# Optimization experiments

Hardware: AMD Instinct MI355X
Metric: run time of the kernel (lower is better)

## Reference

```python
import jax, jax.numpy as jnp
import numpy as np
import math

NHEAD = 8
IOU_THR = 0.2
COS_THR = 0.2


def _build_mask(segments, q):
    # segments: [bz, Lq, 2] (center, length); q: [bz, Lq, d]
    c, l = segments[..., 0], segments[..., 1]
    s, e = c - l / 2, c + l / 2  # ml2se: midpoint-length -> start-end
    inter = jnp.clip(jnp.minimum(e[:, :, None], e[:, None, :])
                     - jnp.maximum(s[:, :, None], s[:, None, :]), 0.0)
    union = l[:, :, None] + l[:, None, :] - inter
    iou = inter / union  # [bz, Lq, Lq]
    qn = q / jnp.maximum(jnp.linalg.norm(q, axis=-1, keepdims=True), 1e-8)
    cos = jnp.einsum('bid,bjd->bij', qn, qn)
    Lq = q.shape[1]
    adj = jnp.broadcast_to(jnp.eye(Lq, dtype=bool), iou.shape)
    adj = jnp.where(iou <= IOU_THR, True, adj)   # adj_matrix[iou<=0.2]=1
    adj = jnp.where(cos <= COS_THR, False, adj)  # adj_matrix[cos<=0.2]=0
    return ~adj  # True = masked


def setup_inputs() -> dict:
    key = jax.random.key(0)
    ks = jax.random.split(key, 8)
    Lq, bz, d = 1024, 8, 512
    bound = 1.0 / math.sqrt(d)
    query = jax.random.normal(ks[0], (Lq, bz, d), jnp.float32)
    segments = jax.random.uniform(ks[1], (bz, Lq, 2), jnp.float32)
    Wq = jax.random.uniform(ks[2], (d, d), jnp.float32, -bound, bound)
    bq = jax.random.uniform(ks[3], (d,), jnp.float32, -bound, bound)
    Wk = jax.random.uniform(ks[4], (d, d), jnp.float32, -bound, bound)
    bk = jax.random.uniform(ks[5], (d,), jnp.float32, -bound, bound)
    Wv = jax.random.uniform(ks[6], (d, d), jnp.float32, -bound, bound)
    bv = jax.random.uniform(ks[7], (d,), jnp.float32, -bound, bound)
    return dict(query=query, segments=segments, Wq=Wq, bq=bq, Wk=Wk, bk=bk,
                Wv=Wv, bv=bv)


def reference(query, segments, Wq, bq, Wk, bk, Wv, bv):
    Lq, bz, d = query.shape
    dh = d // NHEAD
    h = jnp.transpose(query, (1, 0, 2))  # [bz, Lq, d]
    mask = _build_mask(segments, h)      # [bz, Lq, Lq], bool
    Q = (h @ Wq.T + bq).reshape(bz, Lq, NHEAD, dh)
    K = (h @ Wk.T + bk).reshape(bz, Lq, NHEAD, dh)
    V = (h @ Wv.T + bv).reshape(bz, Lq, NHEAD, dh)
    scores = jnp.einsum('bihd,bjhd->bhij', Q, K) / math.sqrt(dh)
    scores = jnp.where(mask[:, None, :, :], -jnp.inf, scores)
    attn = jax.nn.softmax(scores, axis=-1)
    out = jnp.einsum('bhij,bjhd->bihd', attn, V).reshape(bz, Lq, d) + h
    return jnp.transpose(out, (1, 0, 2))  # [Lq, bz, d]
```

## Files before the change

### kernel.cpp

```cpp
#include <hip/hip_runtime.h>
#include <math.h>

#define LQ 1024
#define BZ 8
#define D  512
#define NH 8
#define DH 64
#define IOU_THR 0.2f
#define COS_THR 0.2f
#define NEG (-1e30f)
#define FIXCAP 16384

typedef short bf16x8 __attribute__((ext_vector_type(8)));
typedef float f32x4  __attribute__((ext_vector_type(4)));

#define MFMA16(a, b, cacc) __builtin_amdgcn_mfma_f32_16x16x32_bf16(a, b, cacc, 0, 0, 0)

__device__ inline unsigned short f2bf(float x) {
    union { float f; unsigned int u; } v; v.f = x;
    unsigned int r = v.u + 0x7FFF + ((v.u >> 16) & 1);
    return (unsigned short)(r >> 16);
}

__global__ __launch_bounds__(256) void prep_kernel(const float* __restrict__ query,
                                                   const float* __restrict__ Wq,
                                                   const float* __restrict__ Wk,
                                                   const float* __restrict__ Wv,
                                                   unsigned short* __restrict__ hi,
                                                   unsigned short* __restrict__ Wb,
                                                   float* __restrict__ rnorm) {
    int blk = blockIdx.x, tid = threadIdx.x;
    if (blk < 2048) {
        int w = tid >> 6, lane = tid & 63;
        int row = blk * 4 + w;
        int b = row >> 10, i = row & 1023;
        const float* src = query + ((size_t)i * BZ + b) * D + lane * 8;
        float4 v0 = *(const float4*)src;
        float4 v1 = *(const float4*)(src + 4);
        uint4 pk;
        pk.x = (unsigned)f2bf(v0.x) | ((unsigned)f2bf(v0.y) << 16);
        pk.y = (unsigned)f2bf(v0.z) | ((unsigned)f2bf(v0.w) << 16);
        pk.z = (unsigned)f2bf(v1.x) | ((unsigned)f2bf(v1.y) << 16);
        pk.w = (unsigned)f2bf(v1.z) | ((unsigned)f2bf(v1.w) << 16);
        *(uint4*)(hi + (size_t)row * D + lane * 8) = pk;
        float ss = v0.x * v0.x + v0.y * v0.y + v0.z * v0.z + v0.w * v0.w
                 + v1.x * v1.x + v1.y * v1.y + v1.z * v1.z + v1.w * v1.w;
        #pragma unroll
        for (int s = 1; s < 64; s <<= 1) ss += __shfl_xor(ss, s);
        if (lane == 0) rnorm[row] = 1.0f / fmaxf(sqrtf(ss), 1e-8f);
    } else {
        int t = (blk - 2048) * 256 + tid;
        int mat = t >> 16;
        int off = (t & 65535) * 4;
        const float* src = (mat == 0) ? Wq : (mat == 1) ? Wk : Wv;
        float4 v = *(const float4*)(src + off);
        uint2 p;
        p.x = (unsigned)f2bf(v.x) | ((unsigned)f2bf(v.y) << 16);
        p.y = (unsigned)f2bf(v.z) | ((unsigned)f2bf(v.w) << 16);
        *(uint2*)(Wb + (size_t)mat * D * D + off) = p;
    }
}

__global__ __launch_bounds__(256) void gemm_kernel(const unsigned short* __restrict__ hi,
                                                   const unsigned short* __restrict__ Wb,
                                                   const float* __restrict__ rnorm,
                                                   const float* __restrict__ segments,
                                                   const float* __restrict__ bq,
                                                   const float* __restrict__ bk,
                                                   const float* __restrict__ bv,
                                                   unsigned char* __restrict__ mask,
                                                   unsigned char* __restrict__ summ,
                                                   int* __restrict__ fix_cnt,
                                                   unsigned int* __restrict__ fix_list,
                                                   unsigned short* __restrict__ Qb,
                                                   unsigned short* __restrict__ Kb,
                                                   unsigned short* __restrict__ Vt) {
    __shared__ short As[2][128 * 32], Bs[2][128 * 32];
    __shared__ float4 iSE[128], jSE[128];
    __shared__ int summ_lds[8][2], summ_t_lds[8][2];
    int blk = blockIdx.x, tid = threadIdx.x, w = tid >> 6, lane = tid & 63;
    int c = lane & 15, q4 = lane >> 4;
    int wr = w >> 1, wc = w & 1;

    bool is_qkv = blk < 768;
    const char *Asrc, *Bsrc;
    int b = 0, i0 = 0, j0 = 0, z = 0, m0 = 0, n0 = 0;
    if (is_qkv) {
        z = blk >> 8; int rem = blk & 255;
        m0 = (rem >> 2) * 128; n0 = (rem & 3) * 128;
        Asrc = (const char*)(hi + (size_t)m0 * D);
        Bsrc = (const char*)(Wb + (size_t)z * D * D + (size_t)n0 * D);
    } else {
        int id2 = blk - 768;
        b = id2 / 36;
        int t = id2 - b * 36;
        int it = 0;
        while (t >= 8 - it) { t -= 8 - it; it++; }
        int jt = it + t;
        i0 = it * 128; j0 = jt * 128;
        Asrc = (const char*)(hi + ((size_t)b * LQ + i0) * D);
        Bsrc = (const char*)(hi + ((size_t)b * LQ + j0) * D);
        if (tid < 16) {
            summ_lds[tid >> 1][tid & 1] = 0;
            summ_t_lds[tid >> 1][tid & 1] = 0;
        }
    }

    int lrow = lane >> 2;
    int gl   = (lane & 3) ^ ((lane >> 3) & 3);
    size_t goff = (size_t)lrow * 1024 + (size_t)gl * 16;
    int lds_off = lrow * 64 + (lane & 3) * 16;

    uint4 ra[2], rb[2];
    #pragma unroll
    for (int m = 0; m < 2; m++) {
        int n = 2 * w + m;
        ra[m] = *(const uint4*)(Asrc + (size_t)n * 16384 + goff);
        rb[m] = *(const uint4*)(Bsrc + (size_t)n * 16384 + goff);
    }
    #pragma unroll
    for (int m = 0; m < 2; m++) {
        int n = 2 * w + m;
        *(uint4*)((char*)As[0] + n * 1024 + lds_off) = ra[m];
        *(uint4*)((char*)Bs[0] + n * 1024 + lds_off) = rb[m];
    }
    __syncthreads();

    f32x4 acc[4][4] = {};
    int rswz = (c >> 1) & 3;
    for (int k = 0; k < 16; k++) {
        int cur = k & 1;
        if (k < 15) {
            size_t kb = (size_t)(k + 1) * 64;
            #pragma unroll
            for (int m = 0; m < 2; m++) {
                int n = 2 * w + m;
                ra[m] = *(const uint4*)(Asrc + kb + (size_t)n * 16384 + goff);
                rb[m] = *(const uint4*)(Bsrc + kb + (size_t)n * 16384 + goff);
            }
        }
        bf16x8 af[4], bf[4];
        #pragma unroll
        for (int f = 0; f < 4; f++) {
            af[f] = *(const bf16x8*)&As[cur][(wr * 64 + f * 16 + c) * 32 + (q4 ^ rswz) * 8];
            bf[f] = *(const bf16x8*)&Bs[cur][(wc * 64 + f * 16 + c) * 32 + (q4 ^ rswz) * 8];
        }
        #pragma unroll
        for (int fr = 0; fr < 4; fr++)
            #pragma unroll
            for (int fc = 0; fc < 4; fc++)
                acc[fr][fc] = MFMA16(af[fr], bf[fc], acc[fr][fc]);
        if (k < 15) {
            int nxt = cur ^ 1;
            #pragma unroll
            for (int m = 0; m < 2; m++) {
                int n = 2 * w + m;
                *(uint4*)((char*)As[nxt] + n * 1024 + lds_off) = ra[m];
                *(uint4*)((char*)Bs[nxt] + n * 1024 + lds_off) = rb[m];
            }
        }
        __syncthreads();
    }

    if (is_qkv) {
        const float* bias = (z == 0) ? bq : (z == 1) ? bk : bv;
        #pragma unroll
        for (int fr = 0; fr < 4; fr++)
            #pragma unroll
            for (int r = 0; r < 4; r++) {
                int m = m0 + wr * 64 + fr * 16 + q4 * 4 + r;
                int bb = m >> 10, i = m & 1023;
                #pragma unroll
                for (int fc = 0; fc < 4; fc++) {
                    int n = n0 + wc * 64 + fc * 16 + c;
                    unsigned short us = f2bf(acc[fr][fc][r] + bias[n]);
                    int hh = n >> 6, dh = n & 63;
                    size_t bh = (size_t)bb * NH + hh;
                    if (z == 2)
                        Vt[(bh * DH + dh) * LQ + i] = us;
                    else {
                        unsigned short* dst = (z == 0) ? Qb : Kb;
                        dst[(bh * LQ + i) * DH + dh] = us;
                    }
                }
            }
    } else {
        const float2* seg2 = (const float2*)(segments + (size_t)b * LQ * 2);
        const float* rn = rnorm + b * LQ;
        if (tid < 128) {
            float2 cl = seg2[i0 + tid];
            iSE[tid] = make_float4(cl.x - cl.y * 0.5f, cl.x + cl.y * 0.5f, cl.y, rn[i0 + tid]);
        } else {
            float2 cl = seg2[j0 + tid - 128];
            jSE[tid - 128] = make_float4(cl.x - cl.y * 0.5f, cl.x + cl.y * 0.5f, cl.y, rn[j0 + tid - 128]);
        }
        __syncthreads();

        bool offdiag = (i0 != j0);
        unsigned char* mbase = mask + ((size_t)b << 20);
        int anyT[4] = {0, 0, 0, 0};
        #pragma unroll
        for (int fr = 0; fr < 4; fr++) {
            int anyun = 0;
            unsigned int tpack[4] = {0, 0, 0, 0};
            #pragma unroll
            for (int r = 0; r < 4; r++) {
                int il = wr * 64 + fr * 16 + q4 * 4 + r;
                int i = i0 + il;
                float4 I = iSE[il];
                #pragma unroll
                for (int fc = 0; fc < 4; fc++) {
                    int jl = wc * 64 + fc * 16 + c;
                    int j = j0 + jl;
                    float4 J = jSE[jl];
                    float cosv = acc[fr][fc][r] * I.w * J.w;
                    if (fabsf(cosv - COS_THR) < 1.5e-3f) {
                        int idx = atomicAdd(fix_cnt, 1);
                        if (idx < FIXCAP)
                            fix_list[idx] = ((unsigned int)b << 20) | ((unsigned int)i << 10) | j;
                    }
                    float inter = fmaxf(fminf(I.y, J.y) - fmaxf(I.x, J.x), 0.0f);
                    float uni   = I.z + J.z - inter;
                    float iou   = inter / uni;
                    bool adj = ((iou <= IOU_THR) || (i == j)) && (cosv > COS_THR);
                    mbase[(size_t)i * LQ + j] = adj ? 0 : 1;
                    tpack[fc] |= (adj ? 0u : 1u) << (8 * r);
                    anyun |= adj ? 1 : 0;
                    anyT[fc] |= adj ? 1 : 0;
                }
            }
            if (anyun) atomicOr(&summ_lds[wr * 4 + fr][wc], 1);
            if (offdiag) {
                int ibase = i0 + wr * 64 + fr * 16 + q4 * 4;
                #pragma unroll
                for (int fc = 0; fc < 4; fc++) {
                    int j = j0 + wc * 64 + fc * 16 + c;
                    *(unsigned int*)&mbase[(size_t)j * LQ + ibase] = tpack[fc];
                }
            }
        }
        if (offdiag) {
            #pragma unroll
            for (int fc = 0; fc < 4; fc++)
                if (anyT[fc]) atomicOr(&summ_t_lds[wc * 4 + fc][wr], 1);
        }
        __syncthreads();
        if (tid < 16) {
            int lit = tid >> 1, ljt = tid & 1;
            summ[((size_t)b * 64 + (i0 >> 4) + lit) * 16 + (j0 >> 6) + ljt] =
                summ_lds[lit][ljt] ? 1 : 0;
            if (offdiag)
                summ[((size_t)b * 64 + (j0 >> 4) + lit) * 16 + (i0 >> 6) + ljt] =
                    summ_t_lds[lit][ljt] ? 1 : 0;
        }
    }
}

__global__ __launch_bounds__(64) void fixup_kernel(const float* __restrict__ query,
                                                   const float* __restrict__ rnorm,
                                                   const float* __restrict__ segments,
                                                   const int* __restrict__ fix_cnt,
                                                   const unsigned int* __restrict__ fix_list,
                                                   unsigned char* __restrict__ mask,
                                                   unsigned char* __restrict__ summ) {
    int cnt = *fix_cnt; if (cnt > FIXCAP) cnt = FIXCAP;
    int lane = threadIdx.x;
    for (int e = blockIdx.x; e < cnt; e += gridDim.x) {
        unsigned int pk = fix_list[e];
        int b = pk >> 20, i = (pk >> 10) & 1023, j = pk & 1023;
        const float* hri = query + ((size_t)i * BZ + b) * D;
        const float* hrj = query + ((size_t)j * BZ + b) * D;
        double dd = 0.0;
        #pragma unroll
        for (int k = 0; k < D / 64; k++)
            dd += (double)hri[k * 64 + lane] * (double)hrj[k * 64 + lane];
        #pragma unroll
        for (int s = 1; s < 64; s <<= 1) dd += __shfl_xor(dd, s);
        if (lane == 0) {
            float rni = rnorm[b * LQ + i], rnj = rnorm[b * LQ + j];
            float cosv = (float)(dd * (double)rni * (double)rnj);
            const float* seg = segments + (size_t)b * LQ * 2;
            float ci = seg[i * 2], li = seg[i * 2 + 1];
            float cj = seg[j * 2], lj = seg[j * 2 + 1];
            float si = ci - li * 0.5f, ei = ci + li * 0.5f;
            float sj = cj - lj * 0.5f, ej = cj + lj * 0.5f;
            float inter = fmaxf(fminf(ei, ej) - fmaxf(si, sj), 0.0f);
            float iou = inter / (li + lj - inter);
            bool adj = ((iou <= IOU_THR) || (i == j)) && (cosv > COS_THR);
            unsigned char mv = adj ? 0 : 1;
            mask[((size_t)b * LQ + i) * LQ + j] = mv;
            mask[((size_t)b * LQ + j) * LQ + i] = mv;
            if (adj) {
                summ[((size_t)b * 64 + (i >> 4)) * 16 + (j >> 6)] = 1;
                summ[((size_t)b * 64 + (j >> 4)) * 16 + (i >> 6)] = 1;
            }
        }
    }
}

__global__ __launch_bounds__(256) void attn_kernel(const unsigned short* __restrict__ Qb,
                                                   const unsigned short* __restrict__ Kb,
                                                   const unsigned short* __restrict__ Vt,
                                                   const unsigned char* __restrict__ mask,
                                                   const unsigned char* __restrict__ summ,
                                                   const float* __restrict__ query,
                                                   float* __restrict__ out) {
    int tid = threadIdx.x;
    int w = tid >> 6, lane = tid & 63;
    int c = lane & 15, q4 = lane >> 4;
    int hh = blockIdx.y, b = blockIdx.z;
    int i0 = blockIdx.x * 64 + w * 16;
    size_t bh = (size_t)b * NH + hh;

    __shared__ unsigned short p_lds[4][16][72];

    const unsigned short* Qrow = Qb + (bh * LQ + i0 + c) * DH;
    bf16x8 qa0 = *(const bf16x8*)(Qrow + q4 * 8);
    bf16x8 qa1 = *(const bf16x8*)(Qrow + 32 + q4 * 8);

    f32x4 O[4] = {};
    float m_r[4] = {NEG, NEG, NEG, NEG};
    float l_r[4] = {0.f, 0.f, 0.f, 0.f};

    const unsigned short* Kbase = Kb + bh * LQ * DH;
    const unsigned short* Vbase = Vt + bh * DH * LQ;
    const unsigned char*  mbase = mask + ((size_t)b * LQ + i0) * LQ;
    const unsigned char*  srow  = summ + ((size_t)b * 64 + (i0 >> 4)) * 16;

    for (int jt = 0; jt < 16; jt++) {
        if (!srow[jt]) continue;
        int j0 = jt * 64;
        f32x4 S[4] = {};
        #pragma unroll
        for (int cb = 0; cb < 4; cb++) {
            const unsigned short* krow = Kbase + (size_t)(j0 + cb * 16 + c) * DH;
            bf16x8 kf0 = *(const bf16x8*)(krow + q4 * 8);
            bf16x8 kf1 = *(const bf16x8*)(krow + 32 + q4 * 8);
            S[cb] = MFMA16(qa0, kf0, S[cb]);
            S[cb] = MFMA16(qa1, kf1, S[cb]);
        }
        float p[4][4];
        float tmax[4] = {NEG, NEG, NEG, NEG};
        #pragma unroll
        for (int cb = 0; cb < 4; cb++)
            #pragma unroll
            for (int r = 0; r < 4; r++) {
                float sc = S[cb][r] * 0.125f;
                unsigned char mm = mbase[(size_t)(q4 * 4 + r) * LQ + j0 + cb * 16 + c];
                sc = mm ? NEG : sc;
                p[cb][r] = sc;
                tmax[r] = fmaxf(tmax[r], sc);
            }
        #pragma unroll
        for (int r = 0; r < 4; r++) {
            float v = tmax[r];
            v = fmaxf(v, __shfl_xor(v, 1));
            v = fmaxf(v, __shfl_xor(v, 2));
            v = fmaxf(v, __shfl_xor(v, 4));
            v = fmaxf(v, __shfl_xor(v, 8));
            tmax[r] = v;
        }
        float rsum[4];
        #pragma unroll
        for (int r = 0; r < 4; r++) {
            float mn = fmaxf(m_r[r], tmax[r]);
            float alpha = __expf(m_r[r] - mn);
            m_r[r] = mn;
            l_r[r] *= alpha;
            #pragma unroll
            for (int cb2 = 0; cb2 < 4; cb2++) O[cb2][r] *= alpha;
            float s0 = 0.f;
            #pragma unroll
            for (int cb = 0; cb < 4; cb++) {
                float e = __expf(p[cb][r] - mn);
                p[cb][r] = e;
                s0 += e;
            }
            rsum[r] = s0;
        }
        #pragma unroll
        for (int r = 0; r < 4; r++) {
            float v = rsum[r];
            v += __shfl_xor(v, 1);
            v += __shfl_xor(v, 2);
            v += __shfl_xor(v, 4);
            v += __shfl_xor(v, 8);
            l_r[r] += v;
        }
        #pragma unroll
        for (int cb = 0; cb < 4; cb++)
            #pragma unroll
            for (int r = 0; r < 4; r++)
                p_lds[w][q4 * 4 + r][cb * 16 + c] = f2bf(p[cb][r]);
        #pragma unroll
        for (int s = 0; s < 2; s++) {
            bf16x8 pf = *(const bf16x8*)&p_lds[w][c][s * 32 + q4 * 8];
            #pragma unroll
            for (int cb = 0; cb < 4; cb++) {
                bf16x8 vf = *(const bf16x8*)(Vbase + (size_t)(cb * 16 + c) * LQ + j0 + s * 32 + q4 * 8);
                O[cb] = MFMA16(pf, vf, O[cb]);
            }
        }
    }
    #pragma unroll
    for (int r = 0; r < 4; r++) {
        int i = i0 + q4 * 4 + r;
        float inv = 1.0f / l_r[r];
        #pragma unroll
        for (int cb = 0; cb < 4; cb++) {
            int col = hh * 64 + cb * 16 + c;
            size_t oidx = ((size_t)i * BZ + b) * D + col;
            out[oidx] = O[cb][r] * inv + query[oidx];
        }
    }
}

extern "C" void kernel_launch(void* const* d_in, const int* in_sizes, int n_in,
                              void* d_out, int out_size, void* d_ws, size_t ws_size,
                              hipStream_t stream) {
    const float* query    = (const float*)d_in[0];
    const float* segments = (const float*)d_in[1];
    const float* Wq = (const float*)d_in[2];
    const float* bq = (const float*)d_in[3];
    const float* Wk = (const float*)d_in[4];
    const float* bk = (const float*)d_in[5];
    const float* Wv = (const float*)d_in[6];
    const float* bv = (const float*)d_in[7];
    float* out = (float*)d_out;

    const size_t NTOK = (size_t)BZ * LQ;
    char* ws = (char*)d_ws;
    unsigned short* hbuf  = (unsigned short*)ws;   ws += NTOK * D * 2;
    unsigned short* Qb    = (unsigned short*)ws;   ws += NTOK * D * 2;
    unsigned short* Kb    = (unsigned short*)ws;   ws += NTOK * D * 2;
    unsigned short* Vt    = (unsigned short*)ws;   ws += NTOK * D * 2;
    unsigned short* Wb    = (unsigned short*)ws;   ws += (size_t)3 * D * D * 2;
    float*          rnorm = (float*)ws;            ws += NTOK * 4;
    unsigned char*  mask  = (unsigned char*)ws;    ws += (size_t)BZ * LQ * LQ;
    unsigned char*  summ  = (unsigned char*)ws;    ws += 8192;
    int*            fix_cnt = (int*)ws;            ws += 64;
    unsigned int*   fix_list = (unsigned int*)ws;

    hipMemsetAsync(fix_cnt, 0, 64, stream);
    prep_kernel<<<2816, 256, 0, stream>>>(query, Wq, Wk, Wv, hbuf, Wb, rnorm);
    gemm_kernel<<<1056, 256, 0, stream>>>(hbuf, Wb, rnorm, segments, bq, bk, bv,
                                          mask, summ, fix_cnt, fix_list, Qb, Kb, Vt);
    fixup_kernel<<<64, 64, 0, stream>>>(query, rnorm, segments, fix_cnt, fix_list, mask, summ);
    attn_kernel<<<dim3(LQ / 64, NH, BZ), 256, 0, stream>>>(Qb, Kb, Vt, mask, summ, query, out);
}
```

Before: 159.2 us.

## Stage QKV epilogue through LDS for coalesced 16-byte stores and reorder blocks

The QKV projection epilogue now writes the bf16 tile into a padded shared buffer that reuses the GEMM staging memory, then emits coalesced 16-byte global stores. For V it transposes through LDS so the Vt layout is written as vectors instead of scattered 2-byte stores. Block index mapping is also reordered so consecutive blocks share the same A row tile across Q/K/V and adjacent output tiles, and the mask blocks interleave batches. This adds an extra barrier and LDS traffic in the epilogue.

```diff
diff --git a/kernel.cpp b/kernel.cpp
--- a/kernel.cpp
+++ b/kernel.cpp
@@ -75,9 +75,14 @@
                                                    unsigned short* __restrict__ Qb,
                                                    unsigned short* __restrict__ Kb,
                                                    unsigned short* __restrict__ Vt) {
-    __shared__ short As[2][128 * 32], Bs[2][128 * 32];
+    __shared__ __align__(16) char SMEM[35072];
     __shared__ float4 iSE[128], jSE[128];
     __shared__ int summ_lds[8][2], summ_t_lds[8][2];
+    short* const As0 = (short*)SMEM;
+    short* const As1 = As0 + 4096;
+    short* const Bs0 = As1 + 4096;
+    short* const Bs1 = Bs0 + 4096;
+
     int blk = blockIdx.x, tid = threadIdx.x, w = tid >> 6, lane = tid & 63;
     int c = lane & 15, q4 = lane >> 4;
     int wr = w >> 1, wc = w & 1;
@@ -86,14 +91,17 @@
     const char *Asrc, *Bsrc;
     int b = 0, i0 = 0, j0 = 0, z = 0, m0 = 0, n0 = 0;
     if (is_qkv) {
-        z = blk >> 8; int rem = blk & 255;
-        m0 = (rem >> 2) * 128; n0 = (rem & 3) * 128;
+        int g = (blk & 7) + 8 * ((blk >> 3) / 12);
+        int inner = (blk >> 3) % 12;
+        z = inner >> 2;
+        m0 = g * 128;
+        n0 = (inner & 3) * 128;
         Asrc = (const char*)(hi + (size_t)m0 * D);
         Bsrc = (const char*)(Wb + (size_t)z * D * D + (size_t)n0 * D);
     } else {
-        int id2 = blk - 768;
-        b = id2 / 36;
-        int t = id2 - b * 36;
+        int x = blk - 768;
+        b = x & 7;
+        int t = x >> 3;
         int it = 0;
         while (t >= 8 - it) { t -= 8 - it; it++; }
         int jt = it + t;
@@ -121,15 +129,16 @@
     #pragma unroll
     for (int m = 0; m < 2; m++) {
         int n = 2 * w + m;
-        *(uint4*)((char*)As[0] + n * 1024 + lds_off) = ra[m];
-        *(uint4*)((char*)Bs[0] + n * 1024 + lds_off) = rb[m];
+        *(uint4*)((char*)As0 + n * 1024 + lds_off) = ra[m];
+        *(uint4*)((char*)Bs0 + n * 1024 + lds_off) = rb[m];
     }
     __syncthreads();
 
     f32x4 acc[4][4] = {};
     int rswz = (c >> 1) & 3;
     for (int k = 0; k < 16; k++) {
-        int cur = k & 1;
+        short* Ac = (k & 1) ? As1 : As0;
+        short* Bc = (k & 1) ? Bs1 : Bs0;
         if (k < 15) {
             size_t kb = (size_t)(k + 1) * 64;
             #pragma unroll
@@ -142,8 +151,8 @@
         bf16x8 af[4], bf[4];
         #pragma unroll
         for (int f = 0; f < 4; f++) {
-            af[f] = *(const bf16x8*)&As[cur][(wr * 64 + f * 16 + c) * 32 + (q4 ^ rswz) * 8];
-            bf[f] = *(const bf16x8*)&Bs[cur][(wc * 64 + f * 16 + c) * 32 + (q4 ^ rswz) * 8];
+            af[f] = *(const bf16x8*)&Ac[(wr * 64 + f * 16 + c) * 32 + (q4 ^ rswz) * 8];
+            bf[f] = *(const bf16x8*)&Bc[(wc * 64 + f * 16 + c) * 32 + (q4 ^ rswz) * 8];
         }
         #pragma unroll
         for (int fr = 0; fr < 4; fr++)
@@ -151,12 +160,13 @@
             for (int fc = 0; fc < 4; fc++)
                 acc[fr][fc] = MFMA16(af[fr], bf[fc], acc[fr][fc]);
         if (k < 15) {
-            int nxt = cur ^ 1;
+            short* An = (k & 1) ? As0 : As1;
+            short* Bn = (k & 1) ? Bs0 : Bs1;
             #pragma unroll
             for (int m = 0; m < 2; m++) {
                 int n = 2 * w + m;
-                *(uint4*)((char*)As[nxt] + n * 1024 + lds_off) = ra[m];
-                *(uint4*)((char*)Bs[nxt] + n * 1024 + lds_off) = rb[m];
+                *(uint4*)((char*)An + n * 1024 + lds_off) = ra[m];
+                *(uint4*)((char*)Bn + n * 1024 + lds_off) = rb[m];
             }
         }
         __syncthreads();
@@ -168,22 +178,43 @@
         for (int fr = 0; fr < 4; fr++)
             #pragma unroll
             for (int r = 0; r < 4; r++) {
-                int m = m0 + wr * 64 + fr * 16 + q4 * 4 + r;
-                int bb = m >> 10, i = m & 1023;
+                int row = wr * 64 + fr * 16 + q4 * 4 + r;
+                char* rbase = SMEM + row * 272 + (row >> 3) * 16;
                 #pragma unroll
                 for (int fc = 0; fc < 4; fc++) {
-                    int n = n0 + wc * 64 + fc * 16 + c;
-                    unsigned short us = f2bf(acc[fr][fc][r] + bias[n]);
-                    int hh = n >> 6, dh = n & 63;
-                    size_t bh = (size_t)bb * NH + hh;
-                    if (z == 2)
-                        Vt[(bh * DH + dh) * LQ + i] = us;
-                    else {
-                        unsigned short* dst = (z == 0) ? Qb : Kb;
-                        dst[(bh * LQ + i) * DH + dh] = us;
-                    }
+                    int col = wc * 64 + fc * 16 + c;
+                    *(unsigned short*)(rbase + col * 2) =
+                        f2bf(acc[fr][fc][r] + bias[n0 + col]);
                 }
             }
+        __syncthreads();
+        int bb = m0 >> 10, ib = m0 & 1023;
+        if (z < 2) {
+            unsigned short* dst = (z == 0) ? Qb : Kb;
+            #pragma unroll
+            for (int it2 = 0; it2 < 8; it2++) {
+                int idx = it2 * 256 + tid;
+                int row = idx >> 4, cg = idx & 15;
+                uint4 v = *(const uint4*)(SMEM + row * 272 + (row >> 3) * 16 + cg * 16);
+                int n = n0 + cg * 8;
+                int hh = n >> 6, dh = n & 63;
+                *(uint4*)(dst + (((size_t)bb * NH + hh) * LQ + ib + row) * DH + dh) = v;
+            }
+        } else {
+            #pragma unroll
+            for (int it2 = 0; it2 < 8; it2++) {
+                int idx = it2 * 256 + tid;
+                int rowg = idx & 15, colI = idx >> 4;
+                union { unsigned short s[8]; uint4 v; } u;
+                char* gbase = SMEM + rowg * 16;
+                #pragma unroll
+                for (int rr = 0; rr < 8; rr++)
+                    u.s[rr] = *(const unsigned short*)(gbase + (rowg * 8 + rr) * 272 + colI * 2);
+                int n = n0 + colI;
+                int hh = n >> 6, dh = n & 63;
+                *(uint4*)(Vt + (((size_t)bb * NH + hh) * DH + dh) * LQ + ib + rowg * 8) = u.v;
+            }
+        }
     } else {
         const float2* seg2 = (const float2*)(segments + (size_t)b * LQ * 2);
         const float* rn = rnorm + b * LQ;
```

Result: faster. 150.1 us (-5.7%).
